# Kernel optimization log

Measured on AMD Instinct MI355X. Metric: run time of the kernel, lower is better.

The kernel has to match this reference:

```python
import math
import jax, jax.numpy as jnp
import numpy as np

B, C, H, W = 8, 512, 32, 32
HEADS = 8


def _mix_rot(re, im, Wm, phi):
    # nn.Linear(dim, dim, bias=False) applied channelwise on [B,C,H,W]:
    # y = x @ Wm.T  ->  einsum over input channel c, output channel d
    re2 = jnp.einsum('bchw,dc->bdhw', re, Wm)
    im2 = jnp.einsum('bchw,dc->bdhw', im, Wm)
    c = jnp.cos(phi)[None, :, None, None]
    s = jnp.sin(phi)[None, :, None, None]
    # complex multiply (re2 + i*im2) * (cos phi + i*sin phi)
    return re2 * c - im2 * s, re2 * s + im2 * c


def setup_inputs() -> dict:
    key = jax.random.key(0)
    ks = jax.random.split(key, 6)
    scale = 1.0 / math.sqrt(C)
    return {
        'z_re': jax.random.normal(ks[0], (B, C, H, W), jnp.float32),
        'z_im': jax.random.normal(ks[1], (B, C, H, W), jnp.float32),
        'Wq': jax.random.normal(ks[2], (C, C), jnp.float32) * scale,
        'phi_q': jnp.zeros((C,), jnp.float32),
        'Wk': jax.random.normal(ks[3], (C, C), jnp.float32) * scale,
        'phi_k': jnp.zeros((C,), jnp.float32),
        'Wv': jax.random.normal(ks[4], (C, C), jnp.float32) * scale,
        'phi_v': jnp.zeros((C,), jnp.float32),
        'Wo': jax.random.normal(ks[5], (C, C), jnp.float32) * scale,
        'phi_o': jnp.zeros((C,), jnp.float32),
    }


def reference(z_re, z_im, Wq, phi_q, Wk, phi_k, Wv, phi_v, Wo, phi_o):
    b, c, h, w = z_re.shape
    T = h * w
    dh = c // HEADS

    def tok(a):  # [B,C,H,W] -> [B,T,C]
        return a.reshape(b, c, T).transpose(0, 2, 1)

    qre, qim = _mix_rot(z_re, z_im, Wq, phi_q)
    kre, kim = _mix_rot(z_re, z_im, Wk, phi_k)
    vre, vim = _mix_rot(z_re, z_im, Wv, phi_v)
    qre, qim = tok(qre), tok(qim)
    kre, kim = tok(kre), tok(kim)
    vre, vim = tok(vre), tok(vim)

    # real part of complex inner product: sums over FULL channel dim (no head split)
    scores = (jnp.einsum('btc,buc->btu', qre, kre)
              + jnp.einsum('btc,buc->btu', qim, kim)) / math.sqrt(dh)
    causal = jnp.triu(jnp.ones((T, T), bool), k=1)
    scores = jnp.where(causal[None], -jnp.inf, scores)
    attn = jax.nn.softmax(scores, axis=-1)

    out_re = jnp.einsum('btu,buc->btc', attn, vre)
    out_im = jnp.einsum('btu,buc->btc', attn, vim)

    def grid(a):  # [B,T,C] -> [B,C,H,W]
        return a.transpose(0, 2, 1).reshape(b, c, h, w)

    return _mix_rot(grid(out_re), grid(out_im), Wo, phi_o)
```

## Files before the change

### kernel.cpp

```cpp
#include <hip/hip_runtime.h>
#include <math.h>

#define NB 8
#define NC 512
#define NT 1024
#define BT (NB * NT)
#define SCALE 0.125f
#define NEG_BIG (-3.0e38f)

typedef __attribute__((ext_vector_type(8))) short short8v;
typedef __attribute__((ext_vector_type(8))) _Float16 half8v;
typedef __attribute__((ext_vector_type(4))) float float4v;
#define MFMA_BF16(A, B, C) __builtin_amdgcn_mfma_f32_16x16x32_bf16(A, B, C, 0, 0, 0)
#define MFMA_F16(A, B, C)  __builtin_amdgcn_mfma_f32_16x16x32_f16(A, B, C, 0, 0, 0)

__device__ __forceinline__ ushort f2bf(float f) {
    union { float f; unsigned int i; } v; v.f = f;
    unsigned int r = v.i + 0x7FFFu + ((v.i >> 16) & 1u);
    return (ushort)(r >> 16);
}

__device__ __forceinline__ ushort f2h(float f) {
    return __builtin_bit_cast(unsigned short, (_Float16)f);
}

__device__ __forceinline__ half8v scale8(short8v raw, float s) {
    half8v h = __builtin_bit_cast(half8v, raw);
    const _Float16 hs = (_Float16)s;
    half8v r;
    #pragma unroll
    for (int q = 0; q < 8; ++q) r[q] = h[q] * hs;
    return r;
}

#if defined(__has_builtin)
#if __has_builtin(__builtin_amdgcn_global_load_lds)
#define HAS_GLDS 1
#endif
#endif

#ifdef HAS_GLDS
__device__ __forceinline__ void glds16(const ushort* g, ushort* l) {
    __builtin_amdgcn_global_load_lds(
        (const __attribute__((address_space(1))) unsigned int*)g,
        (__attribute__((address_space(3))) unsigned int*)l, 16, 0, 0);
}
#endif

template<int ROWS>
__device__ __forceinline__ void stage64(const ushort* __restrict__ g, int rsShorts,
                                        ushort* tile, int w, int lane) {
    const int r8 = lane >> 3;
    const int ck = (lane & 7) ^ r8;
    const ushort* gl = g + (size_t)r8 * rsShorts + (ck << 3);
    constexpr int ni = ROWS / 32;
    #pragma unroll
    for (int s = 0; s < ni; ++s) {
        const int issue = w * ni + s;
#ifdef HAS_GLDS
        glds16(gl + (size_t)issue * 8 * rsShorts, tile + issue * 512);
#else
        const uint4 v = *(const uint4*)(gl + (size_t)issue * 8 * rsShorts);
        *(uint4*)(tile + issue * 512 + lane * 8) = v;
#endif
    }
}

__device__ __forceinline__ short8v frag(const ushort* tile, int rr, int q) {
    return *(const short8v*)(tile + rr * 64 + ((q ^ (rr & 7)) << 3));
}

__device__ __forceinline__ int xcd_swz(int flat, int cpx) {
    return (flat & 7) * cpx + (flat >> 3);
}

__global__ __launch_bounds__(256) void prep_zw_kernel(
    const float* __restrict__ zre, const float* __restrict__ zim,
    ushort* __restrict__ Z,
    const float* __restrict__ Wq, const float* __restrict__ Wk,
    const float* __restrict__ Wv, const float* __restrict__ Wo,
    ushort* __restrict__ Wbf)
{
    const int bx = blockIdx.x;
    const int tid = threadIdx.x;
    if (bx >= 2048) {
        const int idx = (bx - 2048) * 256 + tid;
        const int e4 = idx << 2;
        const int m = e4 >> 18;
        const int off = e4 & ((1 << 18) - 1);
        const float* Ws[4] = {Wq, Wk, Wv, Wo};
        const float4 v = *(const float4*)(Ws[m] + off);
        ushort4 o;
        o.x = f2bf(v.x); o.y = f2bf(v.y); o.z = f2bf(v.z); o.w = f2bf(v.w);
        *(ushort4*)(Wbf + ((size_t)m << 18) + off) = o;
        return;
    }
    const int t0 = (bx & 15) << 6, c0 = ((bx >> 4) & 7) << 6;
    const int bz = bx >> 7, b = bz & 7, comp = bz >> 3;
    const float* src = (comp ? zim : zre) + (size_t)b * NC * NT;
    ushort* dst = Z + (size_t)(comp * NB + b) * NT * NC;

    __shared__ ushort T[64][72];
    #pragma unroll
    for (int r = 0; r < 4; ++r) {
        const int cl = (tid >> 4) + r * 16;
        const int t4 = (tid & 15) << 2;
        const float4 v = *(const float4*)(src + (size_t)(c0 + cl) * NT + t0 + t4);
        T[t4 + 0][cl] = f2bf(v.x); T[t4 + 1][cl] = f2bf(v.y);
        T[t4 + 2][cl] = f2bf(v.z); T[t4 + 3][cl] = f2bf(v.w);
    }
    __syncthreads();
    const int tl = tid >> 2, cc = (tid & 3) << 4;
    ushort* op = dst + (size_t)(t0 + tl) * NC + c0 + cc;
    *(uint4*)op       = *(const uint4*)&T[tl][cc];
    *(uint4*)(op + 8) = *(const uint4*)&T[tl][cc + 8];
}

__global__ __launch_bounds__(256, 2) void proj_qk_kernel(
    const ushort* __restrict__ Z, const ushort* __restrict__ Wbf,
    const float* __restrict__ phiq, const float* __restrict__ phik,
    ushort* __restrict__ qre, ushort* __restrict__ qim,
    ushort* __restrict__ kre, ushort* __restrict__ kim)
{
    const int tid = threadIdx.x;
    const int swz = xcd_swz(blockIdx.x + 64 * blockIdx.y, 64);
    const int d0 = (swz & 7) << 6;
    const int m0 = (swz >> 3) << 7;
    const size_t NE = (size_t)BT * NC;

    __shared__ alignas(16) ushort SM[24576];
    ushort* Zr   = SM;
    ushort* Zi   = SM + 8192;
    ushort* Wq_s = SM + 16384;
    ushort* Wk_s = SM + 20480;
    uint*   R    = (uint*)SM;

    float4v accq[2][4][2] = {};
    float4v acck[2][4][2] = {};

    const int w = tid >> 6, lane = tid & 63;
    const int l15 = lane & 15, quad = lane >> 4;
    const int wm = (w & 1) << 6;
    const int wn = (w >> 1) << 5;

    for (int c0 = 0; c0 < NC; c0 += 64) {
        stage64<128>(Z + (size_t)m0 * NC + c0, NC, Zr, w, lane);
        stage64<128>(Z + NE + (size_t)m0 * NC + c0, NC, Zi, w, lane);
        stage64<64>(Wbf + (size_t)d0 * NC + c0, NC, Wq_s, w, lane);
        stage64<64>(Wbf + ((size_t)1 << 18) + (size_t)d0 * NC + c0, NC, Wk_s, w, lane);
        __syncthreads();
        #pragma unroll
        for (int kk = 0; kk < 2; ++kk) {
            const int q0 = kk * 4 + quad;
            short8v zf[2][4], wqf[2], wkf[2];
            #pragma unroll
            for (int i = 0; i < 4; ++i) {
                zf[0][i] = frag(Zr, wm + i * 16 + l15, q0);
                zf[1][i] = frag(Zi, wm + i * 16 + l15, q0);
            }
            #pragma unroll
            for (int j = 0; j < 2; ++j) {
                wqf[j] = frag(Wq_s, wn + j * 16 + l15, q0);
                wkf[j] = frag(Wk_s, wn + j * 16 + l15, q0);
            }
            #pragma unroll
            for (int c = 0; c < 2; ++c)
                #pragma unroll
                for (int i = 0; i < 4; ++i)
                    #pragma unroll
                    for (int j = 0; j < 2; ++j) {
                        accq[c][i][j] = MFMA_BF16(zf[c][i], wqf[j], accq[c][i][j]);
                        acck[c][i][j] = MFMA_BF16(zf[c][i], wkf[j], acck[c][i][j]);
                    }
        }
        __syncthreads();
    }

    float cq[2], sq[2], ck2[2], sk2[2];
    #pragma unroll
    for (int j = 0; j < 2; ++j) {
        const int d = d0 + wn + j * 16 + l15;
        const float pq = phiq[d], pk = phik[d];
        cq[j] = cosf(pq); sq[j] = sinf(pq);
        ck2[j] = cosf(pk); sk2[j] = sinf(pk);
    }
    const int g = tid >> 4, cl = tid & 15;

    #pragma unroll
    for (int j = 0; j < 2; ++j)
        #pragma unroll
        for (int i = 0; i < 4; ++i)
            #pragma unroll
            for (int r = 0; r < 4; ++r) {
                const int row = wm + i * 16 + quad * 4 + r;
                const int col = wn + j * 16 + l15;
                const float ar = accq[0][i][j][r], ai = accq[1][i][j][r];
                R[row * 76 + col] = (uint)f2bf(ar * cq[j] - ai * sq[j])
                                  | ((uint)f2bf(ar * sq[j] + ai * cq[j]) << 16);
            }
    __syncthreads();
    #pragma unroll
    for (int s = 0; s < 8; ++s) {
        const int row = g * 8 + s;
        const uint4 p = *(const uint4*)&R[row * 76 + cl * 4];
        uint2 re, im;
        re.x = (p.x & 0xFFFFu) | (p.y << 16);
        re.y = (p.z & 0xFFFFu) | (p.w << 16);
        im.x = (p.x >> 16) | (p.y & 0xFFFF0000u);
        im.y = (p.z >> 16) | (p.w & 0xFFFF0000u);
        const size_t off = (size_t)(m0 + row) * NC + d0 + cl * 4;
        *(uint2*)(qre + off) = re;
        *(uint2*)(qim + off) = im;
    }
    __syncthreads();

    #pragma unroll
    for (int j = 0; j < 2; ++j)
        #pragma unroll
        for (int i = 0; i < 4; ++i)
            #pragma unroll
            for (int r = 0; r < 4; ++r) {
                const int row = wm + i * 16 + quad * 4 + r;
                const int col = wn + j * 16 + l15;
                const float br = acck[0][i][j][r], bi = acck[1][i][j][r];
                R[row * 76 + col] = (uint)f2bf(br * ck2[j] - bi * sk2[j])
                                  | ((uint)f2bf(br * sk2[j] + bi * ck2[j]) << 16);
            }
    __syncthreads();
    #pragma unroll
    for (int s = 0; s < 8; ++s) {
        const int row = g * 8 + s;
        const uint4 p = *(const uint4*)&R[row * 76 + cl * 4];
        uint2 re, im;
        re.x = (p.x & 0xFFFFu) | (p.y << 16);
        re.y = (p.z & 0xFFFFu) | (p.w << 16);
        im.x = (p.x >> 16) | (p.y & 0xFFFF0000u);
        im.y = (p.z >> 16) | (p.w & 0xFFFF0000u);
        const size_t off = (size_t)(m0 + row) * NC + d0 + cl * 4;
        *(uint2*)(kre + off) = re;
        *(uint2*)(kim + off) = im;
    }
}

__global__ __launch_bounds__(256, 3) void proj_v_kernel(
    const ushort* __restrict__ Z, const ushort* __restrict__ Wbf,
    const float* __restrict__ phiv,
    ushort* __restrict__ vre, ushort* __restrict__ vim)
{
    const int tid = threadIdx.x;
    const int swz = xcd_swz(blockIdx.x + 4 * blockIdx.y, 64);
    const int d0 = (swz & 3) << 7;
    const int bt0 = (swz >> 2) << 6;
    const size_t NE = (size_t)BT * NC;

    __shared__ alignas(16) ushort SM[19456];
    ushort* Wv_s = SM;
    ushort* Zr   = SM + 8192;
    ushort* Zi   = SM + 12288;
    uint*   R    = (uint*)SM;

    float4v acc[2][4][2] = {};

    const int w = tid >> 6, lane = tid & 63;
    const int l15 = lane & 15, quad = lane >> 4;
    const int wm = (w & 1) << 6;
    const int wn = (w >> 1) << 5;

    for (int c0 = 0; c0 < NC; c0 += 64) {
        stage64<128>(Wbf + ((size_t)2 << 18) + (size_t)d0 * NC + c0, NC, Wv_s, w, lane);
        stage64<64>(Z + (size_t)bt0 * NC + c0, NC, Zr, w, lane);
        stage64<64>(Z + NE + (size_t)bt0 * NC + c0, NC, Zi, w, lane);
        __syncthreads();
        #pragma unroll
        for (int kk = 0; kk < 2; ++kk) {
            const int q0 = kk * 4 + quad;
            short8v wvf[4], zf[2][2];
            #pragma unroll
            for (int i = 0; i < 4; ++i)
                wvf[i] = frag(Wv_s, wm + i * 16 + l15, q0);
            #pragma unroll
            for (int j = 0; j < 2; ++j) {
                zf[0][j] = frag(Zr, wn + j * 16 + l15, q0);
                zf[1][j] = frag(Zi, wn + j * 16 + l15, q0);
            }
            #pragma unroll
            for (int c = 0; c < 2; ++c)
                #pragma unroll
                for (int i = 0; i < 4; ++i)
                    #pragma unroll
                    for (int j = 0; j < 2; ++j)
                        acc[c][i][j] = MFMA_BF16(wvf[i], zf[c][j], acc[c][i][j]);
        }
        __syncthreads();
    }

    const int d_own = d0 + wm + (l15 >> 2) * 16 + quad * 4 + (l15 & 3);
    const float ph_own = phiv[d_own];
    const float c_own = cosf(ph_own), s_own = sinf(ph_own);

    #pragma unroll
    for (int i = 0; i < 4; ++i)
        #pragma unroll
        for (int r = 0; r < 4; ++r) {
            const int src = (lane & 48) | (i * 4 + r);
            const float cs = __shfl(c_own, src, 64);
            const float sn = __shfl(s_own, src, 64);
            const int row = wm + i * 16 + quad * 4 + r;
            #pragma unroll
            for (int j = 0; j < 2; ++j) {
                const int col = wn + j * 16 + l15;
                const float vr = acc[0][i][j][r], vi = acc[1][i][j][r];
                R[row * 76 + col] = (uint)f2h(vr * cs - vi * sn)
                                  | ((uint)f2h(vr * sn + vi * cs) << 16);
            }
        }
    __syncthreads();
    const int g = tid >> 4, cl = tid & 15;
    const int b = bt0 >> 10, t0 = bt0 & 1023;
    #pragma unroll
    for (int s = 0; s < 8; ++s) {
        const int row = g * 8 + s;
        const uint4 p = *(const uint4*)&R[row * 76 + cl * 4];
        uint2 re, im;
        re.x = (p.x & 0xFFFFu) | (p.y << 16);
        re.y = (p.z & 0xFFFFu) | (p.w << 16);
        im.x = (p.x >> 16) | (p.y & 0xFFFF0000u);
        im.y = (p.z >> 16) | (p.w & 0xFFFF0000u);
        const size_t off = (size_t)b * NC * NT + (size_t)(d0 + row) * NT + t0 + cl * 4;
        *(uint2*)(vre + off) = re;
        *(uint2*)(vim + off) = im;
    }
}

__global__ __launch_bounds__(256, 2) void scores_kernel(
    const ushort* __restrict__ qre, const ushort* __restrict__ qim,
    const ushort* __restrict__ kre, const ushort* __restrict__ kim,
    ushort* __restrict__ Pp, float2* __restrict__ stats)
{
    const int swz = xcd_swz(blockIdx.x + 8 * (blockIdx.y + 8 * blockIdx.z), 64);
    const int u0b = (swz & 7) << 7;
    const int t0b = (7 - ((swz >> 3) & 7)) << 7;
    if (u0b > t0b) return;
    const int b = swz >> 6;
    const int tid = threadIdx.x;
    const size_t qb = (size_t)b * NT * NC;

    __shared__ alignas(16) ushort SM[32768];
    ushort* Qr = SM;
    ushort* Qi = SM + 8192;
    ushort* Kr = SM + 16384;
    ushort* Ki = SM + 24576;
    ushort* Rs = SM;

    float4v acc[4][4] = {};

    const int w = tid >> 6, lane = tid & 63;
    const int l15 = lane & 15, quad = lane >> 4;
    const int wm = (w & 1) << 6;
    const int wn = (w >> 1) << 6;

    for (int c0 = 0; c0 < NC; c0 += 64) {
        stage64<128>(qre + qb + (size_t)t0b * NC + c0, NC, Qr, w, lane);
        stage64<128>(qim + qb + (size_t)t0b * NC + c0, NC, Qi, w, lane);
        stage64<128>(kre + qb + (size_t)u0b * NC + c0, NC, Kr, w, lane);
        stage64<128>(kim + qb + (size_t)u0b * NC + c0, NC, Ki, w, lane);
        __syncthreads();
        #pragma unroll
        for (int kk = 0; kk < 2; ++kk) {
            const int q0 = kk * 4 + quad;
            short8v qf[2][4], kf[2][4];
            #pragma unroll
            for (int i = 0; i < 4; ++i) {
                qf[0][i] = frag(Qr, wm + i * 16 + l15, q0);
                qf[1][i] = frag(Qi, wm + i * 16 + l15, q0);
                kf[0][i] = frag(Kr, wn + i * 16 + l15, q0);
                kf[1][i] = frag(Ki, wn + i * 16 + l15, q0);
            }
            #pragma unroll
            for (int i = 0; i < 4; ++i)
                #pragma unroll
                for (int j = 0; j < 4; ++j) {
                    acc[i][j] = MFMA_BF16(qf[0][i], kf[0][j], acc[i][j]);
                    acc[i][j] = MFMA_BF16(qf[1][i], kf[1][j], acc[i][j]);
                }
        }
        __syncthreads();
    }

    const int sub = (u0b + wn) >> 6;
    float2* st = stats + (size_t)(b * 16 + sub) * NT;
    #pragma unroll
    for (int i = 0; i < 4; ++i)
        #pragma unroll
        for (int r = 0; r < 4; ++r) {
            const int t = t0b + wm + i * 16 + quad * 4 + r;
            float v[4]; float m = NEG_BIG;
            #pragma unroll
            for (int j = 0; j < 4; ++j) {
                const int u = u0b + wn + j * 16 + l15;
                const float x = (u > t) ? NEG_BIG : acc[i][j][r] * SCALE;
                v[j] = x; m = fmaxf(m, x);
            }
            #pragma unroll
            for (int d = 1; d < 16; d <<= 1) m = fmaxf(m, __shfl_xor(m, d, 64));
            float l = 0.f;
            const int row = wm + i * 16 + quad * 4 + r;
            #pragma unroll
            for (int j = 0; j < 4; ++j) {
                const float e = __expf(v[j] - m);
                l += e;
                Rs[row * 140 + wn + j * 16 + l15] = f2h(e);
            }
            #pragma unroll
            for (int d = 1; d < 16; d <<= 1) l += __shfl_xor(l, d, 64);
            if (l15 == 0) st[t] = make_float2(m, l);
        }
    __syncthreads();
    ushort* Pb = Pp + (size_t)b * NT * NT;
    const int g = tid >> 5, cl = tid & 31;
    #pragma unroll
    for (int s = 0; s < 16; ++s) {
        const int row = g * 16 + s;
        const uint2 p = *(const uint2*)&Rs[row * 140 + cl * 4];
        *(uint2*)(Pb + (size_t)(t0b + row) * NT + u0b + cl * 4) = p;
    }
}

__global__ __launch_bounds__(256, 3) void pv_kernel(
    const ushort* __restrict__ Pp, const float2* __restrict__ stats,
    const ushort* __restrict__ vre, const ushort* __restrict__ vim,
    ushort* __restrict__ Ore, ushort* __restrict__ Oim)
{
    const int swz = xcd_swz(blockIdx.x + 8 * (blockIdx.y + 8 * blockIdx.z), 64);
    const int c0b = (swz & 7) << 6;
    const int t0b = (7 - ((swz >> 3) & 7)) << 7;
    const int b = swz >> 6;
    const int tid = threadIdx.x;
    const ushort* P = Pp + ((size_t)b * NT + t0b) * NT;
    const size_t vb = (size_t)b * NC * NT;
    const int iters = (t0b + 128) >> 6;

    __shared__ alignas(16) ushort SM[20736];
    ushort* Ps = SM;
    ushort* Vr = SM + 8192;
    ushort* Vi = SM + 12288;
    float* sLds = (float*)(SM + 16384);
    uint*  R    = (uint*)SM;

    float4v acc[2][4][2] = {};

    const int w = tid >> 6, lane = tid & 63;
    const int l15 = lane & 15, quad = lane >> 4;
    const int wm = (w & 1) << 6;
    const int wn = (w >> 1) << 5;

    if (tid < 128) {
        const int t = t0b + tid;
        float mv[16], lv[16];
        #pragma unroll
        for (int s = 0; s < 16; ++s) {
            if (s < iters) {
                const float2 v = stats[(size_t)(b * 16 + s) * NT + t];
                mv[s] = v.x; lv[s] = v.y;
            } else { mv[s] = NEG_BIG; lv[s] = 0.f; }
        }
        float M = NEG_BIG;
        #pragma unroll
        for (int s = 0; s < 16; ++s) M = fmaxf(M, mv[s]);
        float L = 0.f; float ev[16];
        #pragma unroll
        for (int s = 0; s < 16; ++s) { ev[s] = __expf(mv[s] - M); L += ev[s] * lv[s]; }
        const float inv = 1.0f / L;
        #pragma unroll
        for (int s = 0; s < 16; ++s) sLds[tid * 17 + s] = ev[s] * inv;
    }

    for (int it = 0; it < iters; ++it) {
        const int u0 = it << 6;
        stage64<128>(P + u0, NT, Ps, w, lane);
        stage64<64>(vre + vb + (size_t)c0b * NT + u0, NT, Vr, w, lane);
        stage64<64>(vim + vb + (size_t)c0b * NT + u0, NT, Vi, w, lane);
        __syncthreads();
        #pragma unroll
        for (int kk = 0; kk < 2; ++kk) {
            const int q0 = kk * 4 + quad;
            half8v pf[4], vf[2][2];
            #pragma unroll
            for (int i = 0; i < 4; ++i) {
                const int row = wm + i * 16 + l15;
                pf[i] = scale8(frag(Ps, row, q0), sLds[row * 17 + it]);
            }
            #pragma unroll
            for (int j = 0; j < 2; ++j) {
                vf[0][j] = __builtin_bit_cast(half8v, frag(Vr, wn + j * 16 + l15, q0));
                vf[1][j] = __builtin_bit_cast(half8v, frag(Vi, wn + j * 16 + l15, q0));
            }
            #pragma unroll
            for (int c = 0; c < 2; ++c)
                #pragma unroll
                for (int i = 0; i < 4; ++i)
                    #pragma unroll
                    for (int j = 0; j < 2; ++j)
                        acc[c][i][j] = MFMA_F16(pf[i], vf[c][j], acc[c][i][j]);
        }
        __syncthreads();
    }

    #pragma unroll
    for (int i = 0; i < 4; ++i)
        #pragma unroll
        for (int j = 0; j < 2; ++j)
            #pragma unroll
            for (int r = 0; r < 4; ++r) {
                const int row = wm + i * 16 + quad * 4 + r;
                const int col = wn + j * 16 + l15;
                R[row * 76 + col] = (uint)f2bf(acc[0][i][j][r])
                                  | ((uint)f2bf(acc[1][i][j][r]) << 16);
            }
    __syncthreads();
    const int g = tid >> 4, cl = tid & 15;
    #pragma unroll
    for (int s = 0; s < 8; ++s) {
        const int row = g * 8 + s;
        const uint4 p = *(const uint4*)&R[row * 76 + cl * 4];
        uint2 re, im;
        re.x = (p.x & 0xFFFFu) | (p.y << 16);
        re.y = (p.z & 0xFFFFu) | (p.w << 16);
        im.x = (p.x >> 16) | (p.y & 0xFFFF0000u);
        im.y = (p.z >> 16) | (p.w & 0xFFFF0000u);
        const size_t off = ((size_t)b * NT + t0b + row) * NC + c0b + cl * 4;
        *(uint2*)(Ore + off) = re;
        *(uint2*)(Oim + off) = im;
    }
}

__global__ __launch_bounds__(256, 3) void proj_out_kernel(
    const ushort* __restrict__ Ore, const ushort* __restrict__ Oim,
    const ushort* __restrict__ Wbf, const float* __restrict__ phio,
    float* __restrict__ outRe, float* __restrict__ outIm)
{
    const int tid = threadIdx.x;
    const int swz = xcd_swz(blockIdx.x + 4 * blockIdx.y, 64);
    const int d0 = (swz & 3) << 7;
    const int bt0 = (swz >> 2) << 6;

    __shared__ alignas(16) ushort SM[19456];
    ushort* Wo_s = SM;
    ushort* Or_s = SM + 8192;
    ushort* Oi_s = SM + 12288;
    float*  Rf   = (float*)SM;

    float4v acc[2][4][2] = {};

    const int w = tid >> 6, lane = tid & 63;
    const int l15 = lane & 15, quad = lane >> 4;
    const int wm = (w & 1) << 6;
    const int wn = (w >> 1) << 5;

    for (int c0 = 0; c0 < NC; c0 += 64) {
        stage64<128>(Wbf + ((size_t)3 << 18) + (size_t)d0 * NC + c0, NC, Wo_s, w, lane);
        stage64<64>(Ore + (size_t)bt0 * NC + c0, NC, Or_s, w, lane);
        stage64<64>(Oim + (size_t)bt0 * NC + c0, NC, Oi_s, w, lane);
        __syncthreads();
        #pragma unroll
        for (int kk = 0; kk < 2; ++kk) {
            const int q0 = kk * 4 + quad;
            short8v wof[4], of[2][2];
            #pragma unroll
            for (int i = 0; i < 4; ++i)
                wof[i] = frag(Wo_s, wm + i * 16 + l15, q0);
            #pragma unroll
            for (int j = 0; j < 2; ++j) {
                of[0][j] = frag(Or_s, wn + j * 16 + l15, q0);
                of[1][j] = frag(Oi_s, wn + j * 16 + l15, q0);
            }
            #pragma unroll
            for (int c = 0; c < 2; ++c)
                #pragma unroll
                for (int i = 0; i < 4; ++i)
                    #pragma unroll
                    for (int j = 0; j < 2; ++j)
                        acc[c][i][j] = MFMA_BF16(wof[i], of[c][j], acc[c][i][j]);
        }
        __syncthreads();
    }

    const int d_own = d0 + wm + (l15 >> 2) * 16 + quad * 4 + (l15 & 3);
    const float ph_own = phio[d_own];
    const float c_own = cosf(ph_own), s_own = sinf(ph_own);
    const int g = tid >> 4, cl = tid & 15;
    const int b = bt0 >> 10, t0 = bt0 & 1023;

    #pragma unroll
    for (int i = 0; i < 4; ++i)
        #pragma unroll
        for (int r = 0; r < 4; ++r) {
            const int src = (lane & 48) | (i * 4 + r);
            const float cs = __shfl(c_own, src, 64);
            const float sn = __shfl(s_own, src, 64);
            const int row = wm + i * 16 + quad * 4 + r;
            #pragma unroll
            for (int j = 0; j < 2; ++j) {
                const int col = wn + j * 16 + l15;
                Rf[row * 76 + col] = acc[0][i][j][r] * cs - acc[1][i][j][r] * sn;
            }
        }
    __syncthreads();
    #pragma unroll
    for (int s = 0; s < 8; ++s) {
        const int row = g * 8 + s;
        const float4 p = *(const float4*)&Rf[row * 76 + cl * 4];
        *(float4*)(outRe + (size_t)b * NC * NT + (size_t)(d0 + row) * NT + t0 + cl * 4) = p;
    }
    __syncthreads();

    #pragma unroll
    for (int i = 0; i < 4; ++i)
        #pragma unroll
        for (int r = 0; r < 4; ++r) {
            const int src = (lane & 48) | (i * 4 + r);
            const float cs = __shfl(c_own, src, 64);
            const float sn = __shfl(s_own, src, 64);
            const int row = wm + i * 16 + quad * 4 + r;
            #pragma unroll
            for (int j = 0; j < 2; ++j) {
                const int col = wn + j * 16 + l15;
                Rf[row * 76 + col] = acc[0][i][j][r] * sn + acc[1][i][j][r] * cs;
            }
        }
    __syncthreads();
    #pragma unroll
    for (int s = 0; s < 8; ++s) {
        const int row = g * 8 + s;
        const float4 p = *(const float4*)&Rf[row * 76 + cl * 4];
        *(float4*)(outIm + (size_t)b * NC * NT + (size_t)(d0 + row) * NT + t0 + cl * 4) = p;
    }
}

extern "C" void kernel_launch(void* const* d_in, const int* in_sizes, int n_in,
                              void* d_out, int out_size, void* d_ws, size_t ws_size,
                              hipStream_t stream) {
    (void)in_sizes; (void)n_in; (void)out_size; (void)ws_size;
    const float* z_re  = (const float*)d_in[0];
    const float* z_im  = (const float*)d_in[1];
    const float* Wq    = (const float*)d_in[2];
    const float* phi_q = (const float*)d_in[3];
    const float* Wk    = (const float*)d_in[4];
    const float* phi_k = (const float*)d_in[5];
    const float* Wv    = (const float*)d_in[6];
    const float* phi_v = (const float*)d_in[7];
    const float* Wo    = (const float*)d_in[8];
    const float* phi_o = (const float*)d_in[9];

    const size_t NE = (size_t)BT * NC;
    ushort* ws  = (ushort*)d_ws;
    ushort* qre = ws + 0 * NE; ushort* qim = ws + 1 * NE;
    ushort* kre = ws + 2 * NE; ushort* kim = ws + 3 * NE;
    ushort* vre = ws + 4 * NE; ushort* vim = ws + 5 * NE;
    ushort* Wbf = ws + 6 * NE;
    ushort* Z  = (ushort*)d_out;
    ushort* Pp = (ushort*)d_out + 2 * NE;
    float2* stats = (float2*)d_out;

    const dim3 blk(256);
    hipLaunchKernelGGL(prep_zw_kernel, dim3(3072), blk, 0, stream,
                       z_re, z_im, Z, Wq, Wk, Wv, Wo, Wbf);
    hipLaunchKernelGGL(proj_qk_kernel, dim3(BT / 128, NC / 64), blk, 0, stream,
                       Z, Wbf, phi_q, phi_k, qre, qim, kre, kim);
    hipLaunchKernelGGL(proj_v_kernel, dim3(NC / 128, BT / 64), blk, 0, stream,
                       Z, Wbf, phi_v, vre, vim);
    hipLaunchKernelGGL(scores_kernel, dim3(NT / 128, NT / 128, NB), blk, 0, stream,
                       qre, qim, kre, kim, Pp, stats);
    hipLaunchKernelGGL(pv_kernel, dim3(NC / 64, NT / 128, NB), blk, 0, stream,
                       Pp, stats, vre, vim, qre, qim);
    hipLaunchKernelGGL(proj_out_kernel, dim3(NC / 128, BT / 64), blk, 0, stream,
                       qre, qim, Wbf, phi_o, (float*)d_out, (float*)d_out + NE);
}
```

Before: 195.6 us.

## Double-buffer LDS staging in scores and PV kernels to overlap loads with MFMA

The scores kernel now splits each channel chunk into separate real and imaginary stages and ping-pongs between two LDS buffers, so the next tile's global loads are issued while MFMAs run on the current one. The PV kernel gets the same double-buffered prefetch of P and V tiles, and the stats-based scale computation overlaps with the first load. This targets the exposed load latency at each synchronisation point. In exchange the PV kernel's LDS footprint roughly doubles and its launch bound drops from 3 to 2 blocks per CU, and the scores kernel now runs twice as many barriers.

```diff
diff --git a/kernel.cpp b/kernel.cpp
--- a/kernel.cpp
+++ b/kernel.cpp
@@ -346,10 +346,6 @@
     const size_t qb = (size_t)b * NT * NC;
 
     __shared__ alignas(16) ushort SM[32768];
-    ushort* Qr = SM;
-    ushort* Qi = SM + 8192;
-    ushort* Kr = SM + 16384;
-    ushort* Ki = SM + 24576;
     ushort* Rs = SM;
 
     float4v acc[4][4] = {};
@@ -359,30 +355,36 @@
     const int wm = (w & 1) << 6;
     const int wn = (w >> 1) << 6;
 
-    for (int c0 = 0; c0 < NC; c0 += 64) {
-        stage64<128>(qre + qb + (size_t)t0b * NC + c0, NC, Qr, w, lane);
-        stage64<128>(qim + qb + (size_t)t0b * NC + c0, NC, Qi, w, lane);
-        stage64<128>(kre + qb + (size_t)u0b * NC + c0, NC, Kr, w, lane);
-        stage64<128>(kim + qb + (size_t)u0b * NC + c0, NC, Ki, w, lane);
-        __syncthreads();
+    stage64<128>(qre + qb + (size_t)t0b * NC, NC, SM, w, lane);
+    stage64<128>(kre + qb + (size_t)u0b * NC, NC, SM + 8192, w, lane);
+    __syncthreads();
+
+    for (int s = 0; s < 16; ++s) {
+        const int cur = (s & 1) << 14;
+        const int nxt = cur ^ 16384;
+        if (s + 1 < 16) {
+            const int c0n = ((s + 1) >> 1) << 6;
+            const ushort* qs = ((s + 1) & 1 ? qim : qre) + qb + (size_t)t0b * NC + c0n;
+            const ushort* ks = ((s + 1) & 1 ? kim : kre) + qb + (size_t)u0b * NC + c0n;
+            stage64<128>(qs, NC, SM + nxt, w, lane);
+            stage64<128>(ks, NC, SM + nxt + 8192, w, lane);
+        }
+        const ushort* Qs = SM + cur;
+        const ushort* Ks = SM + cur + 8192;
         #pragma unroll
         for (int kk = 0; kk < 2; ++kk) {
             const int q0 = kk * 4 + quad;
-            short8v qf[2][4], kf[2][4];
+            short8v qf[4], kf[4];
             #pragma unroll
             for (int i = 0; i < 4; ++i) {
-                qf[0][i] = frag(Qr, wm + i * 16 + l15, q0);
-                qf[1][i] = frag(Qi, wm + i * 16 + l15, q0);
-                kf[0][i] = frag(Kr, wn + i * 16 + l15, q0);
-                kf[1][i] = frag(Ki, wn + i * 16 + l15, q0);
+                qf[i] = frag(Qs, wm + i * 16 + l15, q0);
+                kf[i] = frag(Ks, wn + i * 16 + l15, q0);
             }
             #pragma unroll
             for (int i = 0; i < 4; ++i)
                 #pragma unroll
-                for (int j = 0; j < 4; ++j) {
-                    acc[i][j] = MFMA_BF16(qf[0][i], kf[0][j], acc[i][j]);
-                    acc[i][j] = MFMA_BF16(qf[1][i], kf[1][j], acc[i][j]);
-                }
+                for (int j = 0; j < 4; ++j)
+                    acc[i][j] = MFMA_BF16(qf[i], kf[j], acc[i][j]);
         }
         __syncthreads();
     }
@@ -426,7 +428,7 @@
     }
 }
 
-__global__ __launch_bounds__(256, 3) void pv_kernel(
+__global__ __launch_bounds__(256, 2) void pv_kernel(
     const ushort* __restrict__ Pp, const float2* __restrict__ stats,
     const ushort* __restrict__ vre, const ushort* __restrict__ vim,
     ushort* __restrict__ Ore, ushort* __restrict__ Oim)
@@ -440,11 +442,8 @@
     const size_t vb = (size_t)b * NC * NT;
     const int iters = (t0b + 128) >> 6;
 
-    __shared__ alignas(16) ushort SM[20736];
-    ushort* Ps = SM;
-    ushort* Vr = SM + 8192;
-    ushort* Vi = SM + 12288;
-    float* sLds = (float*)(SM + 16384);
+    __shared__ alignas(16) ushort SM[37120];
+    float* sLds = (float*)(SM + 32768);
     uint*  R    = (uint*)SM;
 
     float4v acc[2][4][2] = {};
@@ -454,6 +453,9 @@
     const int wm = (w & 1) << 6;
     const int wn = (w >> 1) << 5;
 
+    stage64<128>(P, NT, SM, w, lane);
+    stage64<64>(vre + vb + (size_t)c0b * NT, NT, SM + 8192, w, lane);
+    stage64<64>(vim + vb + (size_t)c0b * NT, NT, SM + 12288, w, lane);
     if (tid < 128) {
         const int t = t0b + tid;
         float mv[16], lv[16];
@@ -474,13 +476,20 @@
         #pragma unroll
         for (int s = 0; s < 16; ++s) sLds[tid * 17 + s] = ev[s] * inv;
     }
+    __syncthreads();
 
     for (int it = 0; it < iters; ++it) {
-        const int u0 = it << 6;
-        stage64<128>(P + u0, NT, Ps, w, lane);
-        stage64<64>(vre + vb + (size_t)c0b * NT + u0, NT, Vr, w, lane);
-        stage64<64>(vim + vb + (size_t)c0b * NT + u0, NT, Vi, w, lane);
-        __syncthreads();
+        const int cur = (it & 1) << 14;
+        const int nxt = cur ^ 16384;
+        if (it + 1 < iters) {
+            const int u0 = (it + 1) << 6;
+            stage64<128>(P + u0, NT, SM + nxt, w, lane);
+            stage64<64>(vre + vb + (size_t)c0b * NT + u0, NT, SM + nxt + 8192, w, lane);
+            stage64<64>(vim + vb + (size_t)c0b * NT + u0, NT, SM + nxt + 12288, w, lane);
+        }
+        const ushort* Ps = SM + cur;
+        const ushort* Vr = SM + cur + 8192;
+        const ushort* Vi = SM + cur + 12288;
         #pragma unroll
         for (int kk = 0; kk < 2; ++kk) {
             const int q0 = kk * 4 + quad;
```

Result: faster. 188.4 us (-3.7%).
